# Performance work log

Hardware: AMD Instinct MI355X
Metric: run time of the kernel (lower is better)

Reference implementation:

```python
import jax, jax.numpy as jnp
import numpy as np

C = 512
CTX = 768
HEADS = 8
GROUPS = min(8, C)
EPS = 1e-5


def setup_inputs() -> dict:
    key = jax.random.key(0)
    ks = jax.random.split(key, 10)
    B, H, W, S = 16, 32, 32, 77
    s_in = 1.0 / np.sqrt(C)
    s_ctx = 1.0 / np.sqrt(CTX)
    return {
        "x": jax.random.normal(ks[0], (B, C, H, W), jnp.float32),
        "context": jax.random.normal(ks[1], (B, S, CTX), jnp.float32),
        "gn_w": jnp.ones((C,), jnp.float32),
        "gn_b": jnp.zeros((C,), jnp.float32),
        "q_w": jax.random.normal(ks[2], (C, C), jnp.float32) * s_in,
        "q_b": jnp.zeros((C,), jnp.float32),
        "kv_w": jax.random.normal(ks[3], (2 * C, CTX), jnp.float32) * s_ctx,
        "kv_b": jnp.zeros((2 * C,), jnp.float32),
        "proj_w": jax.random.normal(ks[4], (C, C), jnp.float32) * s_in,
        "proj_b": jnp.zeros((C,), jnp.float32),
    }


def _group_norm(x, w, b):
    # x: [B, C, H, W]; normalize per group over (C/G, H, W)
    B, Cc, H, W = x.shape
    xg = x.reshape(B, GROUPS, Cc // GROUPS, H * W)
    mean = xg.mean(axis=(2, 3), keepdims=True)
    var = xg.var(axis=(2, 3), keepdims=True)
    xn = (xg - mean) * jax.lax.rsqrt(var + EPS)
    xn = xn.reshape(B, Cc, H, W)
    return xn * w[None, :, None, None] + b[None, :, None, None]


def reference(x, context, gn_w, gn_b, q_w, q_b, kv_w, kv_b, proj_w, proj_b):
    B, Cc, H, W = x.shape
    hd = Cc // HEADS
    h = _group_norm(x, gn_w, gn_b).reshape(B, Cc, H * W)
    # 1x1 conv Q == channel-mixing GEMM
    q = jnp.einsum("oc,bcn->bon", q_w, h) + q_b[None, :, None]  # [B, C, HW]
    q = q.reshape(B, HEADS, hd, H * W).transpose(0, 1, 3, 2)      # [B, h, HW, d]
    S = context.shape[1]
    kv = jnp.einsum("bsc,oc->bso", context, kv_w) + kv_b           # [B, S, 2C]
    kv = kv.reshape(B, S, 2, HEADS, hd)
    k = kv[:, :, 0].transpose(0, 2, 1, 3)                          # [B, h, S, d]
    v = kv[:, :, 1].transpose(0, 2, 1, 3)
    scale = hd ** (-0.5)
    attn = jax.nn.softmax(jnp.einsum("bhnd,bhsd->bhns", q, k) * scale, axis=-1)
    out = jnp.einsum("bhns,bhsd->bhnd", attn, v)                   # [B, h, HW, d]
    out = out.transpose(0, 1, 3, 2).reshape(B, Cc, H * W)
    out = jnp.einsum("oc,bcn->bon", proj_w, out) + proj_b[None, :, None]
    return x + out.reshape(B, Cc, H, W)
```

## Files before the change

### kernel.cpp

```cpp
#include <hip/hip_runtime.h>

#define B_   16
#define C_   512
#define HW_  1024
#define S_   77
#define CTX_ 768
#define HEADS_ 8
#define G_   8
#define EPS_ 1e-5f

typedef unsigned short u16;
typedef unsigned int u32;
typedef __attribute__((ext_vector_type(8))) short bfx8;
typedef __attribute__((ext_vector_type(4))) float fx4;

union U2 { u16 h[4]; uint2 v; };

__device__ __forceinline__ u16 f2bf(float f) {
  union { float f; u32 u; } v; v.f = f;
  u32 u = v.u;
  return (u16)((u + 0x7FFFu + ((u >> 16) & 1u)) >> 16);
}

__device__ __forceinline__ void gload16(const u16* g, u16* l) {
  __builtin_amdgcn_global_load_lds((const __attribute__((address_space(1))) u32*)g,
                                   (__attribute__((address_space(3))) u32*)l, 16, 0, 0);
}

__device__ __forceinline__ void castw_body(const float* __restrict__ in,
                                           u16* __restrict__ out, int K, int i, int n4) {
  if (i >= n4) return;
  float4 v = *(const float4*)(in + (size_t)i * 4);
  int K4 = K >> 2;
  int m = i / K4;
  int k = (i - m * K4) * 4;
  int pb = ((k & 63) >> 3) ^ (m & 7);
  size_t dst = (size_t)m * K + (k & ~63) + (pb << 3) + (k & 7);
  U2 pk;
  pk.h[0] = f2bf(v.x); pk.h[1] = f2bf(v.y); pk.h[2] = f2bf(v.z); pk.h[3] = f2bf(v.w);
  *(uint2*)(out + dst) = pk.v;
}

__device__ __forceinline__ void castctx_body(const float* __restrict__ in,
                                             u16* __restrict__ out, int i) {
  if (i >= 16 * 77 * 192) return;
  int rg = i / 192;
  int k = (i - rg * 192) * 4;
  int b = rg / 77, s = rg - b * 77;
  float4 v = *(const float4*)(in + (size_t)i * 4);
  int pb = ((k & 63) >> 3) ^ (s & 7);
  size_t dst = ((size_t)b * 128 + s) * 768 + (k & ~63) + (pb << 3) + (k & 7);
  U2 pk;
  pk.h[0] = f2bf(v.x); pk.h[1] = f2bf(v.y); pk.h[2] = f2bf(v.z); pk.h[3] = f2bf(v.w);
  *(uint2*)(out + dst) = pk.v;
}

__device__ __forceinline__ void gnstats_body(const float* __restrict__ x,
                                             float2* __restrict__ part, int blk, int t) {
  int bg = blk >> 3, slice = blk & 7;
  const float4* x4 = (const float4*)(x + (size_t)bg * 65536);
  float s = 0.f, ss = 0.f;
  #pragma unroll
  for (int j = 0; j < 8; ++j) {
    float4 v = x4[slice * 2048 + j * 256 + t];
    s  += v.x + v.y + v.z + v.w;
    ss += v.x*v.x + v.y*v.y + v.z*v.z + v.w*v.w;
  }
  #pragma unroll
  for (int off = 32; off; off >>= 1) {
    s  += __shfl_down(s, off);
    ss += __shfl_down(ss, off);
  }
  __shared__ float rs[4], rss[4];
  int wid = t >> 6;
  if ((t & 63) == 0) { rs[wid] = s; rss[wid] = ss; }
  __syncthreads();
  if (t == 0)
    part[blk] = make_float2(rs[0] + rs[1] + rs[2] + rs[3],
                            rss[0] + rss[1] + rss[2] + rss[3]);
}

__global__ __launch_bounds__(256) void prep_kernel(const float* __restrict__ q_w,
                                                   const float* __restrict__ kv_w,
                                                   const float* __restrict__ proj_w,
                                                   const float* __restrict__ ctx,
                                                   const float* __restrict__ x,
                                                   u16* __restrict__ qw_bf,
                                                   u16* __restrict__ kvw_bf,
                                                   u16* __restrict__ pjw_bf,
                                                   u16* __restrict__ ctx_bf,
                                                   float2* __restrict__ gpart) {
  int bid = blockIdx.x, t = threadIdx.x;
  if (bid < 256)        castw_body(q_w,    qw_bf,  512, bid * 256 + t, 65536);
  else if (bid < 1024)  castw_body(kv_w,   kvw_bf, 768, (bid - 256) * 256 + t, 196608);
  else if (bid < 1280)  castw_body(proj_w, pjw_bf, 512, (bid - 1024) * 256 + t, 65536);
  else if (bid < 2204)  castctx_body(ctx, ctx_bf, (bid - 1280) * 256 + t);
  else                  gnstats_body(x, gpart, bid - 2204, t);
}

__global__ __launch_bounds__(256) void gn_apply(const float* __restrict__ x,
                                                const float* __restrict__ w,
                                                const float* __restrict__ bgn,
                                                const float2* __restrict__ gpart,
                                                u16* __restrict__ hT) {
  int blk = blockIdx.x;
  int nt = blk & 7, bg = blk >> 3;
  int batch = bg >> 3, g = bg & 7;
  const float4* x4 = (const float4*)(x + ((size_t)batch * C_ + (size_t)g * 64) * HW_);
  float s = 0.f, ss = 0.f;
  #pragma unroll
  for (int j = 0; j < 8; ++j) { float2 pp = gpart[bg * 8 + j]; s += pp.x; ss += pp.y; }
  const float invN = 1.0f / 65536.0f;
  float mean = s * invN;
  float rstd = rsqrtf(ss * invN - mean * mean + EPS_);
  int t = threadIdx.x;
  __shared__ u16 T2[128 * 72];
  int n4i = t & 31;
  int c4b = t >> 5;
  #pragma unroll
  for (int j = 0; j < 2; ++j) {
    int c4 = c4b + j * 8;
    float4 v[4];
    float wcs[4], bcs[4];
    #pragma unroll
    for (int e = 0; e < 4; ++e) {
      int c = c4 * 4 + e;
      v[e] = x4[(size_t)c * 256 + nt * 32 + n4i];
      int cg = g * 64 + c;
      float wc_ = w[cg] * rstd;
      wcs[e] = wc_;
      bcs[e] = bgn[cg] - mean * wc_;
    }
    int cbase = c4 * 4;
    #pragma unroll
    for (int ne = 0; ne < 4; ++ne) {
      int n = n4i * 4 + ne;
      int pb = (cbase >> 3) ^ (n & 7);
      U2 pk;
      pk.h[0] = f2bf(((const float*)&v[0])[ne] * wcs[0] + bcs[0]);
      pk.h[1] = f2bf(((const float*)&v[1])[ne] * wcs[1] + bcs[1]);
      pk.h[2] = f2bf(((const float*)&v[2])[ne] * wcs[2] + bcs[2]);
      pk.h[3] = f2bf(((const float*)&v[3])[ne] * wcs[3] + bcs[3]);
      *(uint2*)&T2[n * 72 + (pb << 3) + (cbase & 7)] = pk.v;
    }
  }
  __syncthreads();
  #pragma unroll
  for (int j = 0; j < 4; ++j) {
    int idx = j * 256 + t;
    int row = idx >> 3, cs = (idx & 7) * 8;
    uint4 vv = *(const uint4*)&T2[row * 72 + cs];
    *(uint4*)(hT + ((size_t)batch * 1024 + nt * 128 + row) * 512 + g * 64 + cs) = vv;
  }
}

__global__ __launch_bounds__(256) void kvgemm_kernel(
    const u16* __restrict__ A, const u16* __restrict__ Bw,
    const float* __restrict__ bias, u16* __restrict__ o16a, u16* __restrict__ o16b)
{
  __shared__ u16 As[64 * 64];
  __shared__ u16 Bs[32 * 64];
  int t = threadIdx.x;
  int b = blockIdx.z;
  int n0 = blockIdx.x * 32, m0 = blockIdx.y * 64;
  const u16* aBase = A + (size_t)b * 98304 + (size_t)(m0 + (t >> 3)) * 768 + (t & 7) * 8;
  const u16* bBase = Bw + (size_t)(n0 + (t >> 3)) * 768 + (t & 7) * 8;
  int wid = t >> 6, l = t & 63;
  int wr = wid & 1, wc = wid >> 1;
  int lr = l & 15, lg = l >> 4, xr = lr & 7;
  fx4 acc[2];
  acc[0] = (fx4){0.f, 0.f, 0.f, 0.f};
  acc[1] = (fx4){0.f, 0.f, 0.f, 0.f};

  for (int k0 = 0; k0 < 768; k0 += 64) {
    __syncthreads();
    #pragma unroll
    for (int i = 0; i < 2; ++i)
      gload16(aBase + k0 + (size_t)i * 32 * 768, As + i * 2048 + t * 8);
    gload16(bBase + k0, Bs + t * 8);
    __syncthreads();
    #pragma unroll
    for (int kk = 0; kk < 2; ++kk) {
      int lb = kk * 4 + lg;
      bfx8 bf = *(const bfx8*)&Bs[(wc * 16 + lr) * 64 + ((lb ^ xr) << 3)];
      #pragma unroll
      for (int mi = 0; mi < 2; ++mi) {
        bfx8 af = *(const bfx8*)&As[(wr * 32 + mi * 16 + lr) * 64 + ((lb ^ xr) << 3)];
        acc[mi] = __builtin_amdgcn_mfma_f32_16x16x32_bf16(af, bf, acc[mi], 0, 0, 0);
      }
    }
  }

  int o = n0 + wc * 16 + lr;
  float bb = bias[o];
  #pragma unroll
  for (int mi = 0; mi < 2; ++mi) {
    int sb = m0 + wr * 32 + mi * 16 + lg * 4;
    if (o < 512) {
      #pragma unroll
      for (int r = 0; r < 4; ++r) {
        int sidx = sb + r;
        if (sidx < 96) {
          int ob = (o & ~63) | (((((o >> 3) & 7) ^ (sidx & 7))) << 3) | (o & 7);
          o16a[(size_t)b * 49152 + (size_t)sidx * 512 + ob] = f2bf(acc[mi][r] + bb);
        }
      }
    } else if (sb < 96) {
      U2 pk;
      #pragma unroll
      for (int r = 0; r < 4; ++r)
        pk.h[r] = (sb + r < S_) ? f2bf(acc[mi][r] + bb) : (u16)0;
      *(uint2*)(o16b + (size_t)b * 49152 + (size_t)(o - 512) * 96 + sb) = pk.v;
    }
  }
}

__global__ __launch_bounds__(256) void gemm2_kernel(
    const u16* __restrict__ A, const u16* __restrict__ Bw,
    const float* __restrict__ bias, const float* __restrict__ resid,
    float* __restrict__ outf, int K, size_t strideA)
{
  __shared__ u16 As[128 * 64];
  __shared__ u16 Bs[128 * 64];
  int t = threadIdx.x;
  int b = blockIdx.z;
  int n0 = blockIdx.x * 128, m0 = blockIdx.y * 128;
  const u16* aBase = A + (size_t)b * strideA + (size_t)(m0 + (t >> 3)) * K + (t & 7) * 8;
  const u16* bBase = Bw + (size_t)(n0 + (t >> 3)) * K + (t & 7) * 8;
  int wid = t >> 6, l = t & 63;
  int wr = wid >> 1, wc = wid & 1;
  int lr = l & 15, lg = l >> 4;
  fx4 acc[4][4];
  #pragma unroll
  for (int i = 0; i < 4; ++i)
    #pragma unroll
    for (int j = 0; j < 4; ++j) acc[i][j] = (fx4){0.f, 0.f, 0.f, 0.f};

  for (int k0 = 0; k0 < K; k0 += 64) {
    __syncthreads();
    #pragma unroll
    for (int i = 0; i < 4; ++i) {
      gload16(aBase + k0 + (size_t)i * 32 * K, As + i * 2048 + t * 8);
      gload16(bBase + k0 + (size_t)i * 32 * K, Bs + i * 2048 + t * 8);
    }
    __syncthreads();
    #pragma unroll
    for (int kk = 0; kk < 2; ++kk) {
      bfx8 af[4], bf[4];
      int xr = (lr & 7);
      #pragma unroll
      for (int i = 0; i < 4; ++i) {
        int lb = kk * 4 + lg;
        af[i] = *(const bfx8*)&As[(wr * 64 + i * 16 + lr) * 64 + ((lb ^ xr) << 3)];
        bf[i] = *(const bfx8*)&Bs[(wc * 64 + i * 16 + lr) * 64 + ((lb ^ xr) << 3)];
      }
      #pragma unroll
      for (int mi = 0; mi < 4; ++mi)
        #pragma unroll
        for (int ni = 0; ni < 4; ++ni)
          acc[mi][ni] = __builtin_amdgcn_mfma_f32_16x16x32_bf16(af[mi], bf[ni], acc[mi][ni], 0, 0, 0);
    }
  }

  float* O = outf + (size_t)b * 524288;
  const float* R = resid + (size_t)b * 524288;
  #pragma unroll
  for (int ni = 0; ni < 4; ++ni) {
    int cc = n0 + wc * 64 + ni * 16 + lr;
    float bb = bias[cc];
    #pragma unroll
    for (int mi = 0; mi < 4; ++mi) {
      size_t off = (size_t)cc * 1024 + m0 + wr * 64 + mi * 16 + lg * 4;
      float4 rv = *(const float4*)(R + off);
      float4 ov;
      ov.x = acc[mi][ni][0] + bb + rv.x;
      ov.y = acc[mi][ni][1] + bb + rv.y;
      ov.z = acc[mi][ni][2] + bb + rv.z;
      ov.w = acc[mi][ni][3] + bb + rv.w;
      *(float4*)(O + off) = ov;
    }
  }
}

__global__ __launch_bounds__(256) void qattn_kernel(const u16* __restrict__ hT,
                                                    const u16* __restrict__ qw,
                                                    const float* __restrict__ q_b,
                                                    const u16* __restrict__ kvK,
                                                    const u16* __restrict__ kvV,
                                                    u16* __restrict__ aoT) {
  __shared__ u16 SH[12288];
  u16* QO = SH;
  u16* As = SH + 4096;
  u16* Bs = SH + 8192;
  u16* Ps = SH + 4096;

  int t = threadIdx.x;
  int n0 = blockIdx.x * 64, head = blockIdx.y, b = blockIdx.z;
  int wid = t >> 6, l = t & 63;
  int lr = l & 15, lg = l >> 4, xr = lr & 7;
  int qbase = wid * 16;

  {
    const u16* aBase = hT + (size_t)b * 524288 + (size_t)(n0 + (t >> 3)) * 512 + (t & 7) * 8;
    const u16* bBase = qw + (size_t)(head * 64 + (t >> 3)) * 512 + (t & 7) * 8;
    fx4 acc[4];
    #pragma unroll
    for (int j = 0; j < 4; ++j) acc[j] = (fx4){0.f, 0.f, 0.f, 0.f};
    for (int k0 = 0; k0 < 512; k0 += 64) {
      __syncthreads();
      #pragma unroll
      for (int i = 0; i < 2; ++i) {
        gload16(aBase + k0 + (size_t)i * 32 * 512, As + i * 2048 + t * 8);
        gload16(bBase + k0 + (size_t)i * 32 * 512, Bs + i * 2048 + t * 8);
      }
      __syncthreads();
      #pragma unroll
      for (int kk = 0; kk < 2; ++kk) {
        int lb = kk * 4 + lg;
        bfx8 af = *(const bfx8*)&As[(qbase + lr) * 64 + ((lb ^ xr) << 3)];
        bfx8 bf[4];
        #pragma unroll
        for (int i = 0; i < 4; ++i)
          bf[i] = *(const bfx8*)&Bs[(i * 16 + lr) * 64 + ((lb ^ xr) << 3)];
        #pragma unroll
        for (int ni = 0; ni < 4; ++ni)
          acc[ni] = __builtin_amdgcn_mfma_f32_16x16x32_bf16(af, bf[ni], acc[ni], 0, 0, 0);
      }
    }
    #pragma unroll
    for (int ni = 0; ni < 4; ++ni) {
      int d = ni * 16 + lr;
      float bb = q_b[head * 64 + d];
      #pragma unroll
      for (int r = 0; r < 4; ++r) {
        int q = qbase + lg * 4 + r;
        QO[q * 64 + ((((d >> 3) ^ (q & 7))) << 3) + (d & 7)] = f2bf(acc[ni][r] + bb);
      }
    }
  }
  __syncthreads();

  {
    int row = qbase + (l >> 2), part = l & 3;
    if (part < 2)
      *(uint4*)&Ps[row * 104 + 80 + part * 8] = (uint4){0u, 0u, 0u, 0u};
  }

  const u16* kB = kvK + (size_t)b * 49152 + head * 64;
  {
    int qrow = qbase + lr;
    fx4 sc[5];
    #pragma unroll
    for (int ti = 0; ti < 5; ++ti) sc[ti] = (fx4){0.f, 0.f, 0.f, 0.f};
    #pragma unroll
    for (int ks = 0; ks < 2; ++ks) {
      int kb = ((ks * 4 + lg) ^ xr) << 3;
      bfx8 a = *(const bfx8*)&QO[qrow * 64 + kb];
      #pragma unroll
      for (int ti = 0; ti < 5; ++ti) {
        bfx8 bb = *(const bfx8*)(kB + (size_t)(ti * 16 + lr) * 512 + kb);
        sc[ti] = __builtin_amdgcn_mfma_f32_16x16x32_bf16(a, bb, sc[ti], 0, 0, 0);
      }
    }
    #pragma unroll
    for (int ti = 0; ti < 5; ++ti) {
      bool valid = (ti * 16 + lr) < S_;
      #pragma unroll
      for (int r = 0; r < 4; ++r)
        sc[ti][r] = valid ? sc[ti][r] * 0.125f : -1e30f;
    }
    fx4 mx = sc[0];
    #pragma unroll
    for (int ti = 1; ti < 5; ++ti)
      #pragma unroll
      for (int r = 0; r < 4; ++r) mx[r] = fmaxf(mx[r], sc[ti][r]);
    #pragma unroll
    for (int off = 1; off < 16; off <<= 1)
      #pragma unroll
      for (int r = 0; r < 4; ++r) mx[r] = fmaxf(mx[r], __shfl_xor(mx[r], off));
    fx4 sm = (fx4){0.f, 0.f, 0.f, 0.f};
    #pragma unroll
    for (int ti = 0; ti < 5; ++ti)
      #pragma unroll
      for (int r = 0; r < 4; ++r) {
        float e = __expf(sc[ti][r] - mx[r]);
        sc[ti][r] = e; sm[r] += e;
      }
    #pragma unroll
    for (int off = 1; off < 16; off <<= 1)
      #pragma unroll
      for (int r = 0; r < 4; ++r) sm[r] += __shfl_xor(sm[r], off);
    #pragma unroll
    for (int ti = 0; ti < 5; ++ti)
      #pragma unroll
      for (int r = 0; r < 4; ++r)
        Ps[(qbase + lg * 4 + r) * 104 + ti * 16 + lr] = f2bf(sc[ti][r] / sm[r]);
  }

  const u16* vB = kvV + (size_t)b * 49152 + (size_t)head * 64 * 96;
  {
    int q = qbase + lr;
    fx4 o[4];
    #pragma unroll
    for (int dt = 0; dt < 4; ++dt) o[dt] = (fx4){0.f, 0.f, 0.f, 0.f};
    #pragma unroll
    for (int ks = 0; ks < 3; ++ks) {
      bfx8 pb_ = *(const bfx8*)&Ps[q * 104 + ks * 32 + lg * 8];
      #pragma unroll
      for (int dt = 0; dt < 4; ++dt) {
        bfx8 a = *(const bfx8*)(vB + (size_t)(dt * 16 + lr) * 96 + ks * 32 + lg * 8);
        o[dt] = __builtin_amdgcn_mfma_f32_16x16x32_bf16(a, pb_, o[dt], 0, 0, 0);
      }
    }
    #pragma unroll
    for (int dt = 0; dt < 4; ++dt) {
      int db = dt * 16 + lg * 4;
      int pb = ((db >> 3) ^ (q & 7));
      U2 pk;
      #pragma unroll
      for (int r = 0; r < 4; ++r) pk.h[r] = f2bf(o[dt][r]);
      *(uint2*)&QO[q * 64 + (pb << 3) + (db & 7)] = pk.v;
    }
  }
  __syncthreads();

  const size_t aobase = (size_t)b * 524288 + (size_t)n0 * 512 + head * 64;
  #pragma unroll
  for (int j = 0; j < 2; ++j) {
    int idx = j * 256 + t;
    int row = idx >> 3, cs = (idx & 7) * 8;
    *(uint4*)(aoT + aobase + (size_t)row * 512 + cs) = *(const uint4*)&QO[row * 64 + cs];
  }
}

extern "C" void kernel_launch(void* const* d_in, const int* in_sizes, int n_in,
                              void* d_out, int out_size, void* d_ws, size_t ws_size,
                              hipStream_t stream) {
  const float* x      = (const float*)d_in[0];
  const float* ctx    = (const float*)d_in[1];
  const float* gn_w   = (const float*)d_in[2];
  const float* gn_b   = (const float*)d_in[3];
  const float* q_w    = (const float*)d_in[4];
  const float* q_b    = (const float*)d_in[5];
  const float* kv_w   = (const float*)d_in[6];
  const float* kv_b   = (const float*)d_in[7];
  const float* proj_w = (const float*)d_in[8];
  const float* proj_b = (const float*)d_in[9];
  float* out = (float*)d_out;

  u16* p = (u16*)d_ws;
  u16* qw_bf  = p; p += 262144;
  u16* kvw_bf = p; p += 786432;
  u16* pjw_bf = p; p += 262144;
  u16* ctx_bf = p; p += 16 * 128 * 768;
  u16* hT     = p; p += 8388608;
  u16* aoT    = p; p += 8388608;
  u16* kvT_k  = p; p += 16 * 96 * 512;
  u16* kvV    = p; p += 16 * 512 * 96;
  float2* gpart = (float2*)p; p += 1024 * 4;

  prep_kernel<<<3228, 256, 0, stream>>>(q_w, kv_w, proj_w, ctx, x,
                                        qw_bf, kvw_bf, pjw_bf, ctx_bf, gpart);

  gn_apply<<<1024, 256, 0, stream>>>(x, gn_w, gn_b, gpart, hT);

  kvgemm_kernel<<<dim3(32, 2, B_), 256, 0, stream>>>(
      ctx_bf, kvw_bf, kv_b, kvT_k, kvV);

  qattn_kernel<<<dim3(16, HEADS_, B_), 256, 0, stream>>>(hT, qw_bf, q_b, kvT_k, kvV, aoT);

  gemm2_kernel<<<dim3(4, 8, B_), 256, 0, stream>>>(
      aoT, pjw_bf, proj_b, x, out, 512, (size_t)1024 * 512);
}
```

Measured before the change: 83.23 us.

## Double-buffer LDS in projection and Q GEMMs; halve projection N-tile

Both the output-projection GEMM and the Q-projection stage inside the attention kernel now use two LDS buffers, issuing the next K-slab's loads before the current slab's MFMAs and keeping one barrier per step. The projection kernel's N-tile shrinks from 128 to 64, which doubles its grid to give more blocks for the 256 CUs. This aims to hide global-load latency and improve occupancy. In exchange LDS use per block grows, which can lower the number of resident blocks, and the smaller projection tile gives less reuse per load.

```diff
diff --git a/kernel.cpp b/kernel.cpp
--- a/kernel.cpp
+++ b/kernel.cpp
@@ -220,53 +220,64 @@
     const float* __restrict__ bias, const float* __restrict__ resid,
     float* __restrict__ outf, int K, size_t strideA)
 {
-  __shared__ u16 As[128 * 64];
-  __shared__ u16 Bs[128 * 64];
+  __shared__ u16 SH[24576];
   int t = threadIdx.x;
   int b = blockIdx.z;
-  int n0 = blockIdx.x * 128, m0 = blockIdx.y * 128;
+  int n0 = blockIdx.x * 64, m0 = blockIdx.y * 128;
   const u16* aBase = A + (size_t)b * strideA + (size_t)(m0 + (t >> 3)) * K + (t & 7) * 8;
   const u16* bBase = Bw + (size_t)(n0 + (t >> 3)) * K + (t & 7) * 8;
   int wid = t >> 6, l = t & 63;
   int wr = wid >> 1, wc = wid & 1;
-  int lr = l & 15, lg = l >> 4;
-  fx4 acc[4][4];
+  int lr = l & 15, lg = l >> 4, xr = lr & 7;
+  fx4 acc[4][2];
   #pragma unroll
   for (int i = 0; i < 4; ++i)
     #pragma unroll
-    for (int j = 0; j < 4; ++j) acc[i][j] = (fx4){0.f, 0.f, 0.f, 0.f};
-
-  for (int k0 = 0; k0 < K; k0 += 64) {
-    __syncthreads();
-    #pragma unroll
-    for (int i = 0; i < 4; ++i) {
-      gload16(aBase + k0 + (size_t)i * 32 * K, As + i * 2048 + t * 8);
-      gload16(bBase + k0 + (size_t)i * 32 * K, Bs + i * 2048 + t * 8);
-    }
-    __syncthreads();
+    for (int j = 0; j < 2; ++j) acc[i][j] = (fx4){0.f, 0.f, 0.f, 0.f};
+
+  #define PSTAGE(k0, buf)                                                      \
+    {                                                                          \
+      u16* As_ = (buf); u16* Bs_ = (buf) + 8192;                               \
+      _Pragma("unroll")                                                        \
+      for (int i = 0; i < 4; ++i)                                              \
+        gload16(aBase + (k0) + (size_t)i * 32 * K, As_ + i * 2048 + t * 8);    \
+      _Pragma("unroll")                                                        \
+      for (int i = 0; i < 2; ++i)                                              \
+        gload16(bBase + (k0) + (size_t)i * 32 * K, Bs_ + i * 2048 + t * 8);    \
+    }
+
+  PSTAGE(0, SH);
+  __syncthreads();
+  int nsteps = K >> 6;
+  for (int step = 0; step < nsteps; ++step) {
+    u16* buf = SH + (step & 1) * 12288;
+    if (step + 1 < nsteps) PSTAGE((step + 1) * 64, SH + ((step + 1) & 1) * 12288);
+    u16* As_ = buf; u16* Bs_ = buf + 8192;
     #pragma unroll
     for (int kk = 0; kk < 2; ++kk) {
-      bfx8 af[4], bf[4];
-      int xr = (lr & 7);
-      #pragma unroll
-      for (int i = 0; i < 4; ++i) {
-        int lb = kk * 4 + lg;
-        af[i] = *(const bfx8*)&As[(wr * 64 + i * 16 + lr) * 64 + ((lb ^ xr) << 3)];
-        bf[i] = *(const bfx8*)&Bs[(wc * 64 + i * 16 + lr) * 64 + ((lb ^ xr) << 3)];
-      }
+      int lb = kk * 4 + lg;
+      bfx8 af[4], bf[2];
+      #pragma unroll
+      for (int i = 0; i < 4; ++i)
+        af[i] = *(const bfx8*)&As_[(wr * 64 + i * 16 + lr) * 64 + ((lb ^ xr) << 3)];
+      #pragma unroll
+      for (int i = 0; i < 2; ++i)
+        bf[i] = *(const bfx8*)&Bs_[(wc * 32 + i * 16 + lr) * 64 + ((lb ^ xr) << 3)];
       #pragma unroll
       for (int mi = 0; mi < 4; ++mi)
         #pragma unroll
-        for (int ni = 0; ni < 4; ++ni)
+        for (int ni = 0; ni < 2; ++ni)
           acc[mi][ni] = __builtin_amdgcn_mfma_f32_16x16x32_bf16(af[mi], bf[ni], acc[mi][ni], 0, 0, 0);
     }
-  }
+    __syncthreads();
+  }
+  #undef PSTAGE
 
   float* O = outf + (size_t)b * 524288;
   const float* R = resid + (size_t)b * 524288;
   #pragma unroll
-  for (int ni = 0; ni < 4; ++ni) {
-    int cc = n0 + wc * 64 + ni * 16 + lr;
+  for (int ni = 0; ni < 2; ++ni) {
+    int cc = n0 + wc * 32 + ni * 16 + lr;
     float bb = bias[cc];
     #pragma unroll
     for (int mi = 0; mi < 4; ++mi) {
@@ -288,10 +299,9 @@
                                                     const u16* __restrict__ kvK,
                                                     const u16* __restrict__ kvV,
                                                     u16* __restrict__ aoT) {
-  __shared__ u16 SH[12288];
+  __shared__ u16 SH[20480];
   u16* QO = SH;
-  u16* As = SH + 4096;
-  u16* Bs = SH + 8192;
+  u16* ST = SH + 4096;
   u16* Ps = SH + 4096;
 
   int t = threadIdx.x;
@@ -303,17 +313,23 @@
   {
     const u16* aBase = hT + (size_t)b * 524288 + (size_t)(n0 + (t >> 3)) * 512 + (t & 7) * 8;
     const u16* bBase = qw + (size_t)(head * 64 + (t >> 3)) * 512 + (t & 7) * 8;
+    #define QSTAGE(k0, buf)                                                    \
+      {                                                                        \
+        gload16(aBase + (k0), (buf) + t * 8);                                  \
+        gload16(aBase + (k0) + (size_t)32 * 512, (buf) + 2048 + t * 8);        \
+        gload16(bBase + (k0), (buf) + 4096 + t * 8);                           \
+        gload16(bBase + (k0) + (size_t)32 * 512, (buf) + 6144 + t * 8);        \
+      }
     fx4 acc[4];
     #pragma unroll
     for (int j = 0; j < 4; ++j) acc[j] = (fx4){0.f, 0.f, 0.f, 0.f};
-    for (int k0 = 0; k0 < 512; k0 += 64) {
-      __syncthreads();
-      #pragma unroll
-      for (int i = 0; i < 2; ++i) {
-        gload16(aBase + k0 + (size_t)i * 32 * 512, As + i * 2048 + t * 8);
-        gload16(bBase + k0 + (size_t)i * 32 * 512, Bs + i * 2048 + t * 8);
-      }
-      __syncthreads();
+    QSTAGE(0, ST);
+    __syncthreads();
+    for (int step = 0; step < 8; ++step) {
+      u16* buf = ST + (step & 1) * 8192;
+      if (step < 7) QSTAGE((step + 1) * 64, ST + ((step + 1) & 1) * 8192);
+      u16* As = buf;
+      u16* Bs = buf + 4096;
       #pragma unroll
       for (int kk = 0; kk < 2; ++kk) {
         int lb = kk * 4 + lg;
@@ -326,7 +342,9 @@
         for (int ni = 0; ni < 4; ++ni)
           acc[ni] = __builtin_amdgcn_mfma_f32_16x16x32_bf16(af, bf[ni], acc[ni], 0, 0, 0);
       }
-    }
+      __syncthreads();
+    }
+    #undef QSTAGE
     #pragma unroll
     for (int ni = 0; ni < 4; ++ni) {
       int d = ni * 16 + lr;
@@ -338,7 +356,6 @@
       }
     }
   }
-  __syncthreads();
 
   {
     int row = qbase + (l >> 2), part = l & 3;
@@ -469,6 +486,6 @@
 
   qattn_kernel<<<dim3(16, HEADS_, B_), 256, 0, stream>>>(hT, qw_bf, q_b, kvT_k, kvV, aoT);
 
-  gemm2_kernel<<<dim3(4, 8, B_), 256, 0, stream>>>(
+  gemm2_kernel<<<dim3(8, 8, B_), 256, 0, stream>>>(
       aoT, pjw_bf, proj_b, x, out, 512, (size_t)1024 * 512);
 }
```

After: 90.85 us. 1.09x slower.

## Split Q projection out of fused attention into a standalone 128x128 GEMM

Applied to the files above, without the earlier changes.

The Q projection was computed inside the attention kernel with small 64x64 tiles. Each (batch, head, query-tile) block reloaded the full 512-wide K slice of hT and qw. It now runs as its own 128x128-tiled MFMA GEMM that writes a bf16 Q tensor, and a slimmer attention kernel loads Q tiles from global memory. This gives better operand reuse and less redundant hT traffic, at the cost of an extra launch and a round trip of Q through memory. aoT reuses the hT buffer.

```diff
diff --git a/kernel.cpp b/kernel.cpp
--- a/kernel.cpp
+++ b/kernel.cpp
@@ -215,6 +215,76 @@
   }
 }
 
+__global__ __launch_bounds__(256) void qgemm_kernel(
+    const u16* __restrict__ A, const u16* __restrict__ Bw,
+    const float* __restrict__ bias, u16* __restrict__ o16a)
+{
+  __shared__ u16 As[128 * 64];
+  __shared__ u16 Bs[128 * 64];
+  int t = threadIdx.x;
+  int b = blockIdx.z;
+  int n0 = blockIdx.x * 128, m0 = blockIdx.y * 128;
+  const u16* aBase = A + (size_t)b * 524288 + (size_t)(m0 + (t >> 3)) * 512 + (t & 7) * 8;
+  const u16* bBase = Bw + (size_t)(n0 + (t >> 3)) * 512 + (t & 7) * 8;
+  int wid = t >> 6, l = t & 63;
+  int wr = wid >> 1, wc = wid & 1;
+  int lr = l & 15, lg = l >> 4, xr = lr & 7;
+  fx4 acc[4][4];
+  #pragma unroll
+  for (int i = 0; i < 4; ++i)
+    #pragma unroll
+    for (int j = 0; j < 4; ++j) acc[i][j] = (fx4){0.f, 0.f, 0.f, 0.f};
+
+  for (int k0 = 0; k0 < 512; k0 += 64) {
+    __syncthreads();
+    #pragma unroll
+    for (int i = 0; i < 4; ++i) {
+      gload16(aBase + k0 + (size_t)i * 32 * 512, As + i * 2048 + t * 8);
+      gload16(bBase + k0 + (size_t)i * 32 * 512, Bs + i * 2048 + t * 8);
+    }
+    __syncthreads();
+    #pragma unroll
+    for (int kk = 0; kk < 2; ++kk) {
+      int lb = kk * 4 + lg;
+      bfx8 af[4], bf[4];
+      #pragma unroll
+      for (int i = 0; i < 4; ++i) {
+        af[i] = *(const bfx8*)&As[(wr * 64 + i * 16 + lr) * 64 + ((lb ^ xr) << 3)];
+        bf[i] = *(const bfx8*)&Bs[(wc * 64 + i * 16 + lr) * 64 + ((lb ^ xr) << 3)];
+      }
+      #pragma unroll
+      for (int mi = 0; mi < 4; ++mi)
+        #pragma unroll
+        for (int ni = 0; ni < 4; ++ni)
+          acc[mi][ni] = __builtin_amdgcn_mfma_f32_16x16x32_bf16(af[mi], bf[ni], acc[mi][ni], 0, 0, 0);
+    }
+  }
+
+  __syncthreads();
+  u16* T = ((wid & 2) ? Bs : As) + (wid & 1) * 4096;
+  #pragma unroll
+  for (int mi = 0; mi < 4; ++mi)
+    #pragma unroll
+    for (int ni = 0; ni < 4; ++ni) {
+      int cl = ni * 16 + lr;
+      float bb = bias[n0 + wc * 64 + cl];
+      #pragma unroll
+      for (int r = 0; r < 4; ++r) {
+        int ml = mi * 16 + lg * 4 + r;
+        int pb = ((cl >> 3) ^ (ml & 7));
+        T[ml * 64 + (pb << 3) + (cl & 7)] = f2bf(acc[mi][ni][r] + bb);
+      }
+    }
+  #pragma unroll
+  for (int j = 0; j < 8; ++j) {
+    int idx = j * 64 + l;
+    int row = idx >> 3, cs = (idx & 7) * 8;
+    uint4 v = *(const uint4*)&T[row * 64 + cs];
+    *(uint4*)(o16a + (size_t)b * 524288 + (size_t)(m0 + wr * 64 + row) * 512
+              + n0 + wc * 64 + cs) = v;
+  }
+}
+
 __global__ __launch_bounds__(256) void gemm2_kernel(
     const u16* __restrict__ A, const u16* __restrict__ Bw,
     const float* __restrict__ bias, const float* __restrict__ resid,
@@ -282,69 +352,28 @@
   }
 }
 
-__global__ __launch_bounds__(256) void qattn_kernel(const u16* __restrict__ hT,
-                                                    const u16* __restrict__ qw,
-                                                    const float* __restrict__ q_b,
-                                                    const u16* __restrict__ kvK,
-                                                    const u16* __restrict__ kvV,
-                                                    u16* __restrict__ aoT) {
-  __shared__ u16 SH[12288];
-  u16* QO = SH;
-  u16* As = SH + 4096;
-  u16* Bs = SH + 8192;
-  u16* Ps = SH + 4096;
-
+__global__ __launch_bounds__(256) void attn_kernel(const u16* __restrict__ qT,
+                                                   const u16* __restrict__ kvK,
+                                                   const u16* __restrict__ kvV,
+                                                   u16* __restrict__ aoT) {
+  __shared__ u16 QO[64 * 64];
+  __shared__ u16 Ps[64 * 104];
   int t = threadIdx.x;
   int n0 = blockIdx.x * 64, head = blockIdx.y, b = blockIdx.z;
   int wid = t >> 6, l = t & 63;
   int lr = l & 15, lg = l >> 4, xr = lr & 7;
   int qbase = wid * 16;
 
-  {
-    const u16* aBase = hT + (size_t)b * 524288 + (size_t)(n0 + (t >> 3)) * 512 + (t & 7) * 8;
-    const u16* bBase = qw + (size_t)(head * 64 + (t >> 3)) * 512 + (t & 7) * 8;
-    fx4 acc[4];
-    #pragma unroll
-    for (int j = 0; j < 4; ++j) acc[j] = (fx4){0.f, 0.f, 0.f, 0.f};
-    for (int k0 = 0; k0 < 512; k0 += 64) {
-      __syncthreads();
-      #pragma unroll
-      for (int i = 0; i < 2; ++i) {
-        gload16(aBase + k0 + (size_t)i * 32 * 512, As + i * 2048 + t * 8);
-        gload16(bBase + k0 + (size_t)i * 32 * 512, Bs + i * 2048 + t * 8);
-      }
-      __syncthreads();
-      #pragma unroll
-      for (int kk = 0; kk < 2; ++kk) {
-        int lb = kk * 4 + lg;
-        bfx8 af = *(const bfx8*)&As[(qbase + lr) * 64 + ((lb ^ xr) << 3)];
-        bfx8 bf[4];
-        #pragma unroll
-        for (int i = 0; i < 4; ++i)
-          bf[i] = *(const bfx8*)&Bs[(i * 16 + lr) * 64 + ((lb ^ xr) << 3)];
-        #pragma unroll
-        for (int ni = 0; ni < 4; ++ni)
-          acc[ni] = __builtin_amdgcn_mfma_f32_16x16x32_bf16(af, bf[ni], acc[ni], 0, 0, 0);
-      }
-    }
-    #pragma unroll
-    for (int ni = 0; ni < 4; ++ni) {
-      int d = ni * 16 + lr;
-      float bb = q_b[head * 64 + d];
-      #pragma unroll
-      for (int r = 0; r < 4; ++r) {
-        int q = qbase + lg * 4 + r;
-        QO[q * 64 + ((((d >> 3) ^ (q & 7))) << 3) + (d & 7)] = f2bf(acc[ni][r] + bb);
-      }
-    }
-  }
-  __syncthreads();
+  const u16* qsrc = qT + (size_t)b * 524288 + (size_t)(n0 + (t >> 3)) * 512 + head * 64 + (t & 7) * 8;
+  gload16(qsrc, QO + t * 8);
+  gload16(qsrc + (size_t)32 * 512, QO + 2048 + t * 8);
 
   {
     int row = qbase + (l >> 2), part = l & 3;
     if (part < 2)
       *(uint4*)&Ps[row * 104 + 80 + part * 8] = (uint4){0u, 0u, 0u, 0u};
   }
+  __syncthreads();
 
   const u16* kB = kvK + (size_t)b * 49152 + head * 64;
   {
@@ -454,10 +483,11 @@
   u16* pjw_bf = p; p += 262144;
   u16* ctx_bf = p; p += 16 * 128 * 768;
   u16* hT     = p; p += 8388608;
-  u16* aoT    = p; p += 8388608;
+  u16* qT     = p; p += 8388608;
   u16* kvT_k  = p; p += 16 * 96 * 512;
   u16* kvV    = p; p += 16 * 512 * 96;
   float2* gpart = (float2*)p; p += 1024 * 4;
+  u16* aoT    = hT;
 
   prep_kernel<<<3228, 256, 0, stream>>>(q_w, kv_w, proj_w, ctx, x,
                                         qw_bf, kvw_bf, pjw_bf, ctx_bf, gpart);
@@ -467,7 +497,9 @@
   kvgemm_kernel<<<dim3(32, 2, B_), 256, 0, stream>>>(
       ctx_bf, kvw_bf, kv_b, kvT_k, kvV);
 
-  qattn_kernel<<<dim3(16, HEADS_, B_), 256, 0, stream>>>(hT, qw_bf, q_b, kvT_k, kvV, aoT);
+  qgemm_kernel<<<dim3(4, 8, B_), 256, 0, stream>>>(hT, qw_bf, q_b, qT);
+
+  attn_kernel<<<dim3(16, HEADS_, B_), 256, 0, stream>>>(qT, kvT_k, kvV, aoT);
 
   gemm2_kernel<<<dim3(4, 8, B_), 256, 0, stream>>>(
       aoT, pjw_bf, proj_b, x, out, 512, (size_t)1024 * 512);
```

Result: slower. 90.56 us (+8.8%).
